# Optimization experiments

Measured on AMD Instinct MI355X. Metric: run time of the kernel, lower is better.

## Reference

```python
import jax, jax.numpy as jnp
import numpy as np


def setup_inputs() -> dict:
    key = jax.random.key(0)
    ks = jax.random.split(key, 8)
    B, D, H, W = 4, 96, 64, 64
    K, N, R = 4, 16, 6
    return {
        "x": jax.random.normal(ks[0], (B, D, H, W), jnp.float32),
        "x_proj_weight": jax.random.normal(ks[1], (K, R + 2 * N, D), jnp.float32) * 0.05,
        "dt_projs_weight": jax.random.normal(ks[2], (K, D, R), jnp.float32) * 0.1,
        "dt_projs_bias": jax.random.normal(ks[3], (K, D), jnp.float32) * 0.1,
        "A_logs": jax.random.uniform(ks[4], (K * D, N), jnp.float32),
        "Ds": jax.random.normal(ks[5], (K * D,), jnp.float32),
        "ln_weight": jnp.ones((D,), jnp.float32),
        "ln_bias": jnp.zeros((D,), jnp.float32),
    }


def reference(x, x_proj_weight, dt_projs_weight, dt_projs_bias, A_logs, Ds, ln_weight, ln_bias):
    B, D, H, W = x.shape
    K, _, R = dt_projs_weight.shape
    N = A_logs.shape[1]
    L = H * W

    # ---- CrossScan: 4 traversal orders (row-major, col-major, and their reverses) ----
    xf = x.reshape(B, D, L)                                   # row-major
    xt = jnp.transpose(x, (0, 1, 3, 2)).reshape(B, D, L)      # col-major
    xs = jnp.stack([xf, xt, xf[..., ::-1], xt[..., ::-1]], axis=1)  # (B, K, D, L)

    # ---- input-dependent projections ----
    x_dbl = jnp.einsum('bkdl,kcd->bkcl', xs, x_proj_weight)   # (B, K, R+2N, L)
    dts, Bs, Cs = jnp.split(x_dbl, [R, R + N], axis=2)        # Bs/Cs: (B, K, N, L)
    dts = jnp.einsum('bkrl,kdr->bkdl', dts, dt_projs_weight)  # (B, K, D, L)

    A = -jnp.exp(A_logs).reshape(K, D, N)                     # (K, D, N)
    delta = jax.nn.softplus(dts + dt_projs_bias[None, :, :, None])  # (B, K, D, L)

    # ---- selective (S6) scan over L ----
    def step(h, inp):
        d_t, u_t, B_t, C_t = inp  # (B,K,D) (B,K,D) (B,K,N) (B,K,N)
        dA = jnp.exp(d_t[..., None] * A[None])                # (B,K,D,N)
        h = h * dA + (d_t * u_t)[..., None] * B_t[:, :, None, :]
        y_t = jnp.einsum('bkdn,bkn->bkd', h, C_t)
        return h, y_t

    h0 = jnp.zeros((B, K, D, N), x.dtype)
    seq = (jnp.moveaxis(delta, -1, 0), jnp.moveaxis(xs, -1, 0),
           jnp.moveaxis(Bs, -1, 0), jnp.moveaxis(Cs, -1, 0))
    _, ys = jax.lax.scan(step, h0, seq)                       # (L, B, K, D)
    ys = jnp.moveaxis(ys, 0, -1)                              # (B, K, D, L)
    ys = ys + Ds.reshape(K, D)[None, :, :, None] * xs         # skip term D*u

    # ---- CrossMerge: undo the 4 traversal orders and sum ----
    m = ys[:, 0:2] + ys[:, 2:4][..., ::-1]                    # (B, 2, D, L)
    y = m[:, 0] + jnp.transpose(m[:, 1].reshape(B, D, W, H), (0, 1, 3, 2)).reshape(B, D, L)

    # ---- out_norm (LayerNorm over channels, v0 path) ----
    y = jnp.transpose(y, (0, 2, 1))                           # (B, L, D)
    mu = y.mean(-1, keepdims=True)
    var = y.var(-1, keepdims=True)
    y = (y - mu) / jnp.sqrt(var + 1e-5) * ln_weight + ln_bias
    return y.reshape(B, H, W, D)
```

## Files before the change

### kernel.cpp

```cpp
#include <hip/hip_runtime.h>
#include <hip/hip_fp16.h>
#include <math.h>

#define B_ 4
#define D_ 96
#define H_ 64
#define W_ 64
#define L_ 4096
#define K_ 4
#define N_ 16
#define R_ 6
#define C_ 38
#define SSX 128
#define CLSX (L_ / SSX)
#define CH_ (B_ * K_ * D_ * N_)

#if defined(__has_builtin)
#if __has_builtin(__builtin_amdgcn_exp2f)
#define EXP2F(x) __builtin_amdgcn_exp2f(x)
#else
#define EXP2F(x) exp2f(x)
#endif
#else
#define EXP2F(x) exp2f(x)
#endif
#define LOG2E 1.44269504f

#define SW(d) ((((d) >> 2) & 7) << 2)

__device__ __forceinline__ int src_idx(int k, int l) {
    int m = (k >= 2) ? (L_ - 1 - l) : l;
    if (k & 1) return ((m & 63) << 6) | (m >> 6);
    return m;
}

__device__ __forceinline__ float softplus_f(float a) {
    return (a > 15.f) ? a : __logf(1.f + __expf(a));
}

__device__ __forceinline__ ushort f2h(float v) {
    return __half_as_ushort(__float2half_rn(v));
}

__device__ __forceinline__ void load_h8(const __half* p, float* out) {
    uint4 raw = *(const uint4*)p;
    const __half2* h2 = (const __half2*)&raw;
#pragma unroll
    for (int i = 0; i < 4; ++i) {
        float2 f = __half22float2(h2[i]);
        out[2 * i] = f.x;
        out[2 * i + 1] = f.y;
    }
}

__device__ __forceinline__ void store_h8(__half* p, const float* v) {
    uint4 raw;
    __half2* h2 = (__half2*)&raw;
#pragma unroll
    for (int i = 0; i < 4; ++i)
        h2[i] = __floats2half2_rn(v[2 * i], v[2 * i + 1]);
    *(uint4*)p = raw;
}

__device__ __forceinline__ float4 load_h4(const __half* p) {
    uint2 raw = *(const uint2*)p;
    const __half2* h2 = (const __half2*)&raw;
    float2 a = __half22float2(h2[0]);
    float2 b = __half22float2(h2[1]);
    return make_float4(a.x, a.y, b.x, b.y);
}

__global__ __launch_bounds__(256) void transpose_kernel(
    const float* __restrict__ x,
    __half* __restrict__ xs2)
{
    int bid = blockIdx.x;
    int b = bid / (3 * 64);
    int rest = bid % (3 * 64);
    int dblk = rest / 64, lblk = rest % 64;
    int d0 = dblk * 32;
    int l0 = lblk * 64;
    int tid = threadIdx.x;

    __shared__ float s_t[32][65];

    for (int i = tid; i < 32 * 64; i += 256) {
        int d = i >> 6, l = i & 63;
        s_t[d][l] = x[((long)b * D_ + d0 + d) * L_ + l0 + l];
    }
    __syncthreads();

    for (int i = tid; i < 64 * 32; i += 256) {
        int l = i >> 5, d = i & 31;
        __half v = __float2half_rn(s_t[d][l]);
        xs2[((long)b * L_ + l0 + l) * D_ + d0 + d] = v;
        xs2[((long)(B_ + b) * L_ + l * 64 + lblk) * D_ + d0 + d] = v;
    }
}

__global__ __launch_bounds__(256) void proj_scan_kernel(
    const __half* __restrict__ xs2,
    const float* __restrict__ xpw,
    const float* __restrict__ wdt,
    const float* __restrict__ bdt,
    const float* __restrict__ A_logs,
    __half* __restrict__ delta,
    __half* __restrict__ Bsb,
    __half* __restrict__ Csb,
    __half* __restrict__ pAarr,
    __half* __restrict__ hharr)
{
    const int TL = 64;
    const int tiles = L_ / TL;
    int bid = blockIdx.x;
    int bk = bid / tiles;
    int tile = bid % tiles;
    int b = bk / K_, k = bk % K_;
    int l0 = tile * TL;
    int tid = threadIdx.x;

    __shared__ __align__(16) float  s_wpT[D_ * 40];
    __shared__ __align__(16) __half s_xs[D_ * 68];
    __shared__ __align__(16) float  s_wdt[R_ * D_];
    __shared__ __align__(16) float  s_bias[D_];
    __shared__ __align__(16) float  s_dts[R_ * 68];
    __shared__ __align__(16) float  s_B[TL * N_];

    for (int i = tid; i < C_ * D_; i += 256) {
        int d = i / C_, c = i % C_;
        int cp = (c < 6) ? c : c + 2;
        s_wpT[d * 40 + cp] = xpw[(k * C_ + c) * D_ + d];
    }
    for (int i = tid; i < 96; i += 256) {
        s_wpT[i * 40 + 6] = 0.f;
        s_wpT[i * 40 + 7] = 0.f;
    }
    for (int i = tid; i < R_ * D_; i += 256) {
        int r = i / D_, d = i % D_;
        s_wdt[i] = wdt[(k * D_ + d) * R_ + r];
    }
    if (tid < D_) s_bias[tid] = bdt[k * D_ + tid];

    const __half* xsp = xs2 + (long)((k & 1) * B_ + b) * L_ * D_;
    for (int i = tid; i < TL * 24; i += 256) {
        int lt = i / 24, dq = i % 24;
        int row = (k < 2) ? (l0 + lt) : (L_ - 1 - l0 - lt);
        uint2 raw = *(const uint2*)(xsp + (long)row * D_ + dq * 4);
        const __half* hv = (const __half*)&raw;
        int d0 = dq * 4;
        s_xs[(d0 + 0) * 68 + (lt ^ SW(d0 + 0))] = hv[0];
        s_xs[(d0 + 1) * 68 + (lt ^ SW(d0 + 1))] = hv[1];
        s_xs[(d0 + 2) * 68 + (lt ^ SW(d0 + 2))] = hv[2];
        s_xs[(d0 + 3) * 68 + (lt ^ SW(d0 + 3))] = hv[3];
    }
    __syncthreads();

    long base = (long)bk * L_ + l0;

    int ct = tid >> 4;
    int lt4 = (tid & 15) * 4;
    if (ct < 10) {
        int cp0 = ct * 4;
        float acc[4][4];
#pragma unroll
        for (int i = 0; i < 4; ++i)
#pragma unroll
            for (int j = 0; j < 4; ++j) acc[i][j] = 0.f;
#pragma unroll 4
        for (int d = 0; d < D_; ++d) {
            float4 wv = *(const float4*)(&s_wpT[d * 40 + cp0]);
            float4 xv = load_h4(&s_xs[d * 68 + (lt4 ^ SW(d))]);
            float wa[4] = {wv.x, wv.y, wv.z, wv.w};
            float xa[4] = {xv.x, xv.y, xv.z, xv.w};
#pragma unroll
            for (int ci = 0; ci < 4; ++ci)
#pragma unroll
                for (int li = 0; li < 4; ++li)
                    acc[ci][li] += wa[ci] * xa[li];
        }
        if (ct == 0) {
#pragma unroll
            for (int ci = 0; ci < 4; ++ci)
                *(float4*)(&s_dts[ci * 68 + lt4]) =
                    make_float4(acc[ci][0], acc[ci][1], acc[ci][2], acc[ci][3]);
        } else if (ct == 1) {
#pragma unroll
            for (int ci = 0; ci < 2; ++ci)
                *(float4*)(&s_dts[(4 + ci) * 68 + lt4]) =
                    make_float4(acc[ci][0], acc[ci][1], acc[ci][2], acc[ci][3]);
        } else if (ct < 6) {
            int n0 = cp0 - 8;
#pragma unroll
            for (int li = 0; li < 4; ++li) {
                ushort4 hv;
                hv.x = f2h(acc[0][li]); hv.y = f2h(acc[1][li]);
                hv.z = f2h(acc[2][li]); hv.w = f2h(acc[3][li]);
                *(ushort4*)(&Bsb[(base + lt4 + li) * N_ + n0]) = hv;
                *(float4*)(&s_B[(lt4 + li) * N_ + n0]) =
                    make_float4(acc[0][li], acc[1][li], acc[2][li], acc[3][li]);
            }
        } else {
            int n0 = cp0 - 24;
#pragma unroll
            for (int li = 0; li < 4; ++li) {
                ushort4 hv;
                hv.x = f2h(acc[0][li]); hv.y = f2h(acc[1][li]);
                hv.z = f2h(acc[2][li]); hv.w = f2h(acc[3][li]);
                *(ushort4*)(&Csb[(base + lt4 + li) * N_ + n0]) = hv;
            }
        }
    }
    __syncthreads();

    for (int tt = tid; tt < 24 * 16; tt += 256) {
        int dt = tt % 24, lt4b = (tt / 24) * 4;
        int d0 = dt * 4;
        float4 bias = *(const float4*)(&s_bias[d0]);
        float acc[4][4];
#pragma unroll
        for (int li = 0; li < 4; ++li) {
            acc[li][0] = bias.x; acc[li][1] = bias.y;
            acc[li][2] = bias.z; acc[li][3] = bias.w;
        }
#pragma unroll
        for (int r = 0; r < R_; ++r) {
            float4 wv = *(const float4*)(&s_wdt[r * D_ + d0]);
            float4 tv = *(const float4*)(&s_dts[r * 68 + lt4b]);
            float wa[4] = {wv.x, wv.y, wv.z, wv.w};
            float ta[4] = {tv.x, tv.y, tv.z, tv.w};
#pragma unroll
            for (int li = 0; li < 4; ++li)
#pragma unroll
                for (int di = 0; di < 4; ++di)
                    acc[li][di] += ta[li] * wa[di];
        }
#pragma unroll
        for (int li = 0; li < 4; ++li) {
            ushort4 o;
            o.x = f2h(softplus_f(acc[li][0]));
            o.y = f2h(softplus_f(acc[li][1]));
            o.z = f2h(softplus_f(acc[li][2]));
            o.w = f2h(softplus_f(acc[li][3]));
            *(ushort4*)(&delta[(base + lt4b + li) * D_ + d0]) = o;
        }
    }

    if (tid < 192) {
        int sub = tid / 96;
        int dd = tid % 96;
        int j = tile * 2 + sub;
        int kd = k * D_ + dd;

        float A2[16];
        {
            const float4* ap = (const float4*)(A_logs + kd * N_);
#pragma unroll
            for (int q = 0; q < 4; ++q) {
                float4 a = ap[q];
                A2[q * 4 + 0] = -__expf(a.x) * LOG2E;
                A2[q * 4 + 1] = -__expf(a.y) * LOG2E;
                A2[q * 4 + 2] = -__expf(a.z) * LOG2E;
                A2[q * 4 + 3] = -__expf(a.w) * LOG2E;
            }
        }
        float wdtr[R_];
#pragma unroll
        for (int r = 0; r < R_; ++r) wdtr[r] = s_wdt[r * D_ + dd];
        float biasv = s_bias[dd];
        int sw = SW(dd);

        float h[16];
#pragma unroll
        for (int i = 0; i < 16; ++i) h[i] = 0.f;
        float sdel = 0.f;

#pragma unroll 4
        for (int t = 0; t < CLSX; ++t) {
            int lt = sub * CLSX + t;
            float acc = biasv;
#pragma unroll
            for (int r = 0; r < R_; ++r) acc += wdtr[r] * s_dts[r * 68 + lt];
            float del = softplus_f(acc);
            float u = __half2float(s_xs[dd * 68 + (lt ^ sw)]);
            float Bv[16];
            *(float4*)(Bv + 0)  = *(const float4*)(&s_B[lt * N_ + 0]);
            *(float4*)(Bv + 4)  = *(const float4*)(&s_B[lt * N_ + 4]);
            *(float4*)(Bv + 8)  = *(const float4*)(&s_B[lt * N_ + 8]);
            *(float4*)(Bv + 12) = *(const float4*)(&s_B[lt * N_ + 12]);
            sdel += del;
            float delu = del * u;
#pragma unroll
            for (int i = 0; i < 16; ++i) {
                float dA = EXP2F(del * A2[i]);
                h[i] = h[i] * dA + delu * Bv[i];
            }
        }

        long sbase = (long)j * CH_ + (long)(bk * D_ + dd) * N_;
        float pv[16];
#pragma unroll
        for (int i = 0; i < 16; ++i) pv[i] = EXP2F(A2[i] * sdel);
        store_h8(pAarr + sbase, pv);
        store_h8(pAarr + sbase + 8, pv + 8);
        store_h8(hharr + sbase, h);
        store_h8(hharr + sbase + 8, h + 8);
    }
}

__global__ __launch_bounds__(256) void scan_combine(
    const __half* __restrict__ pAarr,
    __half* __restrict__ hharr)
{
    int c = blockIdx.x * 256 + threadIdx.x;
    float h = 0.f;
#pragma unroll 16
    for (int j = 0; j < SSX; ++j) {
        long idx = (long)j * CH_ + c;
        float tmp = __half2float(hharr[idx]);
        float pa  = __half2float(pAarr[idx]);
        hharr[idx] = __float2half_rn(h);
        h = tmp + pa * h;
    }
}

__global__ __launch_bounds__(384) void scan_part2_pair(
    const float* __restrict__ A_logs,
    const float* __restrict__ Ds,
    const __half* __restrict__ xs2,
    const __half* __restrict__ delta,
    const __half* __restrict__ Bsb,
    const __half* __restrict__ Csb,
    const __half* __restrict__ hharr,
    float* __restrict__ ypair)
{
    __shared__ float s_y[2][CLSX][D_];

    int bid = blockIdx.x;
    int b = bid / (2 * SSX);
    int rest = bid % (2 * SSX);
    int p = rest / SSX;
    int j = rest % SSX;
    int tid = threadIdx.x;
    int g = tid / 192;
    int r = tid % 192;
    int dd = r >> 1;
    int half = r & 1;
    int n0 = half * 8;

    int kdir = p + 2 * g;
    int bk = b * K_ + kdir;
    int jj = g ? (SSX - 1 - j) : j;
    int l0s = jj * CLSX;
    int kd = kdir * D_ + dd;

    float A2[8];
    {
        const float4* ap = (const float4*)(A_logs + kd * N_ + n0);
        float4 a0 = ap[0], a1 = ap[1];
        A2[0] = -__expf(a0.x) * LOG2E; A2[1] = -__expf(a0.y) * LOG2E;
        A2[2] = -__expf(a0.z) * LOG2E; A2[3] = -__expf(a0.w) * LOG2E;
        A2[4] = -__expf(a1.x) * LOG2E; A2[5] = -__expf(a1.y) * LOG2E;
        A2[6] = -__expf(a1.z) * LOG2E; A2[7] = -__expf(a1.w) * LOG2E;
    }
    float Dv = Ds[kd];

    const __half* dp = delta + ((long)bk * L_ + l0s) * D_ + dd;
    const __half* bp = Bsb + ((long)bk * L_ + l0s) * N_ + n0;
    const __half* cp = Csb + ((long)bk * L_ + l0s) * N_ + n0;
    const __half* xsp = xs2 + (long)(p * B_ + b) * L_ * D_;
    long urow0 = g ? ((long)j * CLSX + CLSX - 1) : (long)l0s;
    long ustep = g ? -D_ : D_;
    const __half* up = xsp + urow0 * D_ + dd;

    float h[8];
    load_h8(hharr + (long)jj * CH_ + (long)(bk * D_ + dd) * N_ + n0, h);

#pragma unroll 4
    for (int t = 0; t < CLSX; ++t) {
        float del = __half2float(dp[(long)t * D_]);
        float u   = __half2float(up[(long)t * ustep]);
        float Bv[8], Cv[8];
        load_h8(bp + t * N_, Bv);
        load_h8(cp + t * N_, Cv);
        float delu = del * u;
        float yv = 0.f;
#pragma unroll
        for (int i = 0; i < 8; ++i) {
            float dA = EXP2F(del * A2[i]);
            h[i] = h[i] * dA + delu * Bv[i];
            yv += h[i] * Cv[i];
        }
        yv += __shfl_xor(yv, 1);
        if (half == 0) {
            int tpos = g ? (CLSX - 1 - t) : t;
            s_y[g][tpos][dd] = yv + Dv * u;
        }
    }
    __syncthreads();

    float* yo = ypair + ((long)(p * B_ + b) * L_ + (long)j * CLSX) * D_;
    for (int i = tid; i < CLSX * 24; i += 384) {
        int lt = i / 24, dq = i % 24;
        int d0 = dq * 4;
        float4 o = make_float4(s_y[0][lt][d0 + 0] + s_y[1][lt][d0 + 0],
                               s_y[0][lt][d0 + 1] + s_y[1][lt][d0 + 1],
                               s_y[0][lt][d0 + 2] + s_y[1][lt][d0 + 2],
                               s_y[0][lt][d0 + 3] + s_y[1][lt][d0 + 3]);
        *(float4*)(yo + (long)lt * D_ + d0) = o;
    }
}

__global__ __launch_bounds__(256) void ln_merge_kernel(
    const float* __restrict__ ypair,
    const float* __restrict__ lnw,
    const float* __restrict__ lnb,
    float* __restrict__ out)
{
    int wid = (blockIdx.x * 256 + threadIdx.x) >> 6;
    int lane = threadIdx.x & 63;
    int b = wid / L_;
    int m = wid % L_;
    int mt = ((m & 63) << 6) | (m >> 6);

    const float* y0 = ypair + ((long)b * L_ + m) * D_;
    const float* y1 = ypair + ((long)(B_ + b) * L_ + mt) * D_;

    float v0 = y0[lane] + y1[lane];
    float v1 = (lane < 32) ? (y0[64 + lane] + y1[64 + lane]) : 0.f;

    float s  = v0 + v1;
    float s2 = v0 * v0 + v1 * v1;
#pragma unroll
    for (int mm = 1; mm < 64; mm <<= 1) {
        s  += __shfl_xor(s, mm);
        s2 += __shfl_xor(s2, mm);
    }
    float mu  = s * (1.f / D_);
    float var = s2 * (1.f / D_) - mu * mu;
    float rstd = rsqrtf(var + 1e-5f);

    long obase = (long)wid * D_;
    out[obase + lane] = (v0 - mu) * rstd * lnw[lane] + lnb[lane];
    if (lane < 32)
        out[obase + 64 + lane] = (v1 - mu) * rstd * lnw[64 + lane] + lnb[64 + lane];
}

__global__ __launch_bounds__(256) void proj_legacy(
    const float* __restrict__ x,
    const float* __restrict__ xpw,
    const float* __restrict__ wdt,
    const float* __restrict__ bdt,
    float* __restrict__ delta,
    float* __restrict__ Bsb,
    float* __restrict__ Csb)
{
    const int TL = 64;
    const int tiles = L_ / TL;
    int bid = blockIdx.x;
    int bk = bid / tiles;
    int tile = bid % tiles;
    int b = bk / K_, k = bk % K_;
    int l0 = tile * TL;
    int tid = threadIdx.x;

    __shared__ float s_wp[C_ * D_];
    __shared__ float s_wdt[R_ * D_];
    __shared__ float s_bias[D_];
    __shared__ float s_xs[D_ * (TL + 1)];
    __shared__ float s_xdbl[C_ * (TL + 1)];

    for (int i = tid; i < C_ * D_; i += 256) s_wp[i] = xpw[k * C_ * D_ + i];
    for (int i = tid; i < R_ * D_; i += 256) {
        int r = i / D_, d = i % D_;
        s_wdt[i] = wdt[(k * D_ + d) * R_ + r];
    }
    if (tid < D_) s_bias[tid] = bdt[k * D_ + tid];
    for (int i = tid; i < D_ * TL; i += 256) {
        int d = i / TL, lt = i % TL;
        s_xs[d * (TL + 1) + lt] = x[(b * D_ + d) * L_ + src_idx(k, l0 + lt)];
    }
    __syncthreads();

    for (int idx = tid; idx < C_ * TL; idx += 256) {
        int c = idx / TL, lt = idx % TL;
        const float* wr = &s_wp[c * D_];
        float acc = 0.f;
#pragma unroll 8
        for (int d = 0; d < D_; ++d) acc += wr[d] * s_xs[d * (TL + 1) + lt];
        s_xdbl[c * (TL + 1) + lt] = acc;
    }
    __syncthreads();

    long base = (long)bk * L_ + l0;
    for (int idx = tid; idx < TL * D_; idx += 256) {
        int lt = idx / D_, d = idx % D_;
        float acc = s_bias[d];
#pragma unroll
        for (int r = 0; r < R_; ++r)
            acc += s_wdt[r * D_ + d] * s_xdbl[r * (TL + 1) + lt];
        delta[(base + lt) * D_ + d] = softplus_f(acc);
    }
    for (int idx = tid; idx < TL * 2 * N_; idx += 256) {
        int lt = idx / (2 * N_), c2 = idx % (2 * N_);
        float v = s_xdbl[(R_ + c2) * (TL + 1) + lt];
        if (c2 < N_) Bsb[(base + lt) * N_ + c2] = v;
        else         Csb[(base + lt) * N_ + (c2 - N_)] = v;
    }
}

__global__ __launch_bounds__(64) void scan_serial(
    const float* __restrict__ x,
    const float* __restrict__ A_logs,
    const float* __restrict__ Ds,
    const float* __restrict__ delta,
    const float* __restrict__ Bsb,
    const float* __restrict__ Csb,
    float* __restrict__ ys)
{
    const int chans = D_ / 4;
    int bid = blockIdx.x;
    int bk = bid / chans;
    int d0 = (bid % chans) * 4;
    int b = bk / K_, k = bk % K_;
    int lane = threadIdx.x;
    int g = lane >> 4, n = lane & 15;
    int d = d0 + g;
    int kd = k * D_ + d;

    float A  = -__expf(A_logs[kd * N_ + n]);
    float Dv = Ds[kd];
    const float* dptr = delta + ((long)bk * L_) * D_ + d;
    const float* bptr = Bsb + (long)bk * L_ * N_ + n;
    const float* cptr = Csb + (long)bk * L_ * N_ + n;
    const float* xptr = x + ((long)b * D_ + d) * L_;
    float* yptr = ys + ((long)bk * L_) * D_ + d;

    float h = 0.f;
#pragma unroll 4
    for (int l = 0; l < L_; ++l) {
        float del = dptr[(long)l * D_];
        float u   = xptr[src_idx(k, l)];
        float Bt  = bptr[l * N_];
        float Ct  = cptr[l * N_];
        float dA  = __expf(del * A);
        h = h * dA + del * u * Bt;
        float yv = h * Ct;
        yv += __shfl_xor(yv, 1);
        yv += __shfl_xor(yv, 2);
        yv += __shfl_xor(yv, 4);
        yv += __shfl_xor(yv, 8);
        if (n == 0) yptr[(long)l * D_] = yv + Dv * u;
    }
}

__global__ __launch_bounds__(256) void merge_ln_kernel(
    const float* __restrict__ ys,
    const float* __restrict__ lnw,
    const float* __restrict__ lnb,
    float* __restrict__ out)
{
    int wid = (blockIdx.x * 256 + threadIdx.x) >> 6;
    int lane = threadIdx.x & 63;
    int b = wid / L_;
    int l = wid % L_;
    int lt = ((l & 63) << 6) | (l >> 6);

    long base0 = ((long)(b * K_ + 0) * L_ + l) * D_;
    long base2 = ((long)(b * K_ + 2) * L_ + (L_ - 1 - l)) * D_;
    long base1 = ((long)(b * K_ + 1) * L_ + lt) * D_;
    long base3 = ((long)(b * K_ + 3) * L_ + (L_ - 1 - lt)) * D_;

    int dA = lane;
    int dB = lane + 64;
    float v0 = ys[base0 + dA] + ys[base2 + dA] + ys[base1 + dA] + ys[base3 + dA];
    float v1 = 0.f;
    if (dB < D_)
        v1 = ys[base0 + dB] + ys[base2 + dB] + ys[base1 + dB] + ys[base3 + dB];

    float s  = v0 + v1;
    float s2 = v0 * v0 + v1 * v1;
#pragma unroll
    for (int m = 1; m < 64; m <<= 1) {
        s  += __shfl_xor(s, m);
        s2 += __shfl_xor(s2, m);
    }
    float mu  = s * (1.f / D_);
    float var = s2 * (1.f / D_) - mu * mu;
    float rstd = rsqrtf(var + 1e-5f);

    long obase = ((long)b * L_ + l) * D_;
    out[obase + dA] = (v0 - mu) * rstd * lnw[dA] + lnb[dA];
    if (dB < D_)
        out[obase + dB] = (v1 - mu) * rstd * lnw[dB] + lnb[dB];
}

extern "C" void kernel_launch(void* const* d_in, const int* in_sizes, int n_in,
                              void* d_out, int out_size, void* d_ws, size_t ws_size,
                              hipStream_t stream) {
    const float* x      = (const float*)d_in[0];
    const float* xpw    = (const float*)d_in[1];
    const float* wdt    = (const float*)d_in[2];
    const float* bdt    = (const float*)d_in[3];
    const float* A_logs = (const float*)d_in[4];
    const float* Ds     = (const float*)d_in[5];
    const float* lnw    = (const float*)d_in[6];
    const float* lnb    = (const float*)d_in[7];
    float* out = (float*)d_out;

    const long n_delta = (long)B_ * K_ * L_ * D_;
    const long n_bc    = (long)B_ * K_ * L_ * N_;
    const long n_bld   = (long)B_ * L_ * D_;
    const long n_sum   = (long)SSX * CH_;

    char* wsb = (char*)d_ws;
    __half* delta = (__half*)wsb;
    __half* Bsb   = (__half*)(wsb + n_delta * 2);
    __half* Csb   = (__half*)(wsb + n_delta * 2 + n_bc * 2);
    __half* xs2   = (__half*)(wsb + n_delta * 2 + n_bc * 4);
    float*  ypair = (float*)(wsb + n_delta * 2 + n_bc * 4 + 2 * n_bld * 2);
    __half* hharr = (__half*)((char*)ypair + 2 * n_bld * 4);
    __half* pAarr = (__half*)ypair;
    size_t need = (size_t)(n_delta * 2 + n_bc * 4 + 2 * n_bld * 2) +
                  (size_t)(2 * n_bld) * 4 + (size_t)n_sum * 2;

    if (ws_size >= need) {
        transpose_kernel<<<B_ * 3 * 64, 256, 0, stream>>>(x, xs2);
        proj_scan_kernel<<<B_ * K_ * (L_ / 64), 256, 0, stream>>>(
            xs2, xpw, wdt, bdt, A_logs, delta, Bsb, Csb, pAarr, hharr);
        scan_combine<<<CH_ / 256, 256, 0, stream>>>(pAarr, hharr);
        scan_part2_pair<<<B_ * 2 * SSX, 384, 0, stream>>>(
            A_logs, Ds, xs2, delta, Bsb, Csb, hharr, ypair);
        ln_merge_kernel<<<(B_ * L_) / 4, 256, 0, stream>>>(ypair, lnw, lnb, out);
    } else {
        float* ws = (float*)d_ws;
        float* deltaf = ws;
        float* Bsb2   = deltaf + n_delta;
        float* Csb2   = Bsb2 + n_bc;
        float* ys2    = Csb2 + n_bc;
        proj_legacy<<<B_ * K_ * (L_ / 64), 256, 0, stream>>>(
            x, xpw, wdt, bdt, deltaf, Bsb2, Csb2);
        scan_serial<<<B_ * K_ * (D_ / 4), 64, 0, stream>>>(
            x, A_logs, Ds, deltaf, Bsb2, Csb2, ys2);
        merge_ln_kernel<<<(B_ * L_) / 4, 256, 0, stream>>>(ys2, lnw, lnb, out);
    }
}
```

Measured before the change: 170.5 us.

## Split chunk-state combine into hierarchical three-pass scan and store ypair as fp16

The single serial combine kernel, which launched only 96 blocks each walking all 128 chunks, becomes three passes. The first reduces groups of 32 chunks into per-group (A, B) pairs. The second scans the four group pairs. The third replays each group from its prefix to write the chunk-start states. This raises block-level parallelism for the latency-bound combine, at the cost of an extra read pass over pAarr/hharr and two extra launches. Separately, the merged per-direction outputs (ypair) are stored in fp16 instead of fp32, halving that intermediate's write and read traffic in the scan and layer-norm kernels but adding rounding error before LayerNorm.

```diff
diff --git a/kernel.cpp b/kernel.cpp
--- a/kernel.cpp
+++ b/kernel.cpp
@@ -14,6 +14,8 @@
 #define SSX 128
 #define CLSX (L_ / SSX)
 #define CH_ (B_ * K_ * D_ * N_)
+#define GRP_ 4
+#define GJ_ (SSX / GRP_)
 
 #if defined(__has_builtin)
 #if __has_builtin(__builtin_amdgcn_exp2f)
@@ -307,19 +309,60 @@
     }
 }
 
-__global__ __launch_bounds__(256) void scan_combine(
+__global__ __launch_bounds__(256) void combine_c1(
     const __half* __restrict__ pAarr,
-    __half* __restrict__ hharr)
+    const __half* __restrict__ hharr,
+    float* __restrict__ gA,
+    float* __restrict__ gB)
+{
+    int g = blockIdx.x / 96;
+    int c = (blockIdx.x % 96) * 256 + threadIdx.x;
+    long base = (long)g * GJ_ * CH_ + c;
+    float A = 1.f, Bc = 0.f;
+#pragma unroll 8
+    for (int j = 0; j < GJ_; ++j) {
+        long idx = base + (long)j * CH_;
+        float a = __half2float(pAarr[idx]);
+        float b = __half2float(hharr[idx]);
+        A = a * A;
+        Bc = a * Bc + b;
+    }
+    gA[(long)g * CH_ + c] = A;
+    gB[(long)g * CH_ + c] = Bc;
+}
+
+__global__ __launch_bounds__(256) void combine_c2(
+    const float* __restrict__ gA,
+    float* __restrict__ gB)
 {
     int c = blockIdx.x * 256 + threadIdx.x;
     float h = 0.f;
-#pragma unroll 16
-    for (int j = 0; j < SSX; ++j) {
-        long idx = (long)j * CH_ + c;
-        float tmp = __half2float(hharr[idx]);
-        float pa  = __half2float(pAarr[idx]);
+#pragma unroll
+    for (int g = 0; g < GRP_; ++g) {
+        long idx = (long)g * CH_ + c;
+        float A = gA[idx];
+        float Bc = gB[idx];
+        gB[idx] = h;
+        h = A * h + Bc;
+    }
+}
+
+__global__ __launch_bounds__(256) void combine_c3(
+    const __half* __restrict__ pAarr,
+    const float* __restrict__ gB,
+    __half* __restrict__ hharr)
+{
+    int g = blockIdx.x / 96;
+    int c = (blockIdx.x % 96) * 256 + threadIdx.x;
+    long base = (long)g * GJ_ * CH_ + c;
+    float h = gB[(long)g * CH_ + c];
+#pragma unroll 8
+    for (int j = 0; j < GJ_; ++j) {
+        long idx = base + (long)j * CH_;
+        float a = __half2float(pAarr[idx]);
+        float b = __half2float(hharr[idx]);
         hharr[idx] = __float2half_rn(h);
-        h = tmp + pa * h;
+        h = b + a * h;
     }
 }
 
@@ -331,7 +374,7 @@
     const __half* __restrict__ Bsb,
     const __half* __restrict__ Csb,
     const __half* __restrict__ hharr,
-    float* __restrict__ ypair)
+    __half* __restrict__ ypair)
 {
     __shared__ float s_y[2][CLSX][D_];
 
@@ -398,20 +441,21 @@
     }
     __syncthreads();
 
-    float* yo = ypair + ((long)(p * B_ + b) * L_ + (long)j * CLSX) * D_;
+    __half* yo = ypair + ((long)(p * B_ + b) * L_ + (long)j * CLSX) * D_;
     for (int i = tid; i < CLSX * 24; i += 384) {
         int lt = i / 24, dq = i % 24;
         int d0 = dq * 4;
-        float4 o = make_float4(s_y[0][lt][d0 + 0] + s_y[1][lt][d0 + 0],
-                               s_y[0][lt][d0 + 1] + s_y[1][lt][d0 + 1],
-                               s_y[0][lt][d0 + 2] + s_y[1][lt][d0 + 2],
-                               s_y[0][lt][d0 + 3] + s_y[1][lt][d0 + 3]);
-        *(float4*)(yo + (long)lt * D_ + d0) = o;
+        ushort4 o;
+        o.x = f2h(s_y[0][lt][d0 + 0] + s_y[1][lt][d0 + 0]);
+        o.y = f2h(s_y[0][lt][d0 + 1] + s_y[1][lt][d0 + 1]);
+        o.z = f2h(s_y[0][lt][d0 + 2] + s_y[1][lt][d0 + 2]);
+        o.w = f2h(s_y[0][lt][d0 + 3] + s_y[1][lt][d0 + 3]);
+        *(ushort4*)(yo + (long)lt * D_ + d0) = o;
     }
 }
 
 __global__ __launch_bounds__(256) void ln_merge_kernel(
-    const float* __restrict__ ypair,
+    const __half* __restrict__ ypair,
     const float* __restrict__ lnw,
     const float* __restrict__ lnb,
     float* __restrict__ out)
@@ -422,11 +466,12 @@
     int m = wid % L_;
     int mt = ((m & 63) << 6) | (m >> 6);
 
-    const float* y0 = ypair + ((long)b * L_ + m) * D_;
-    const float* y1 = ypair + ((long)(B_ + b) * L_ + mt) * D_;
-
-    float v0 = y0[lane] + y1[lane];
-    float v1 = (lane < 32) ? (y0[64 + lane] + y1[64 + lane]) : 0.f;
+    const __half* y0 = ypair + ((long)b * L_ + m) * D_;
+    const __half* y1 = ypair + ((long)(B_ + b) * L_ + mt) * D_;
+
+    float v0 = __half2float(y0[lane]) + __half2float(y1[lane]);
+    float v1 = (lane < 32)
+        ? (__half2float(y0[64 + lane]) + __half2float(y1[64 + lane])) : 0.f;
 
     float s  = v0 + v1;
     float s2 = v0 * v0 + v1 * v1;
@@ -617,17 +662,22 @@
     __half* Bsb   = (__half*)(wsb + n_delta * 2);
     __half* Csb   = (__half*)(wsb + n_delta * 2 + n_bc * 2);
     __half* xs2   = (__half*)(wsb + n_delta * 2 + n_bc * 4);
-    float*  ypair = (float*)(wsb + n_delta * 2 + n_bc * 4 + 2 * n_bld * 2);
-    __half* hharr = (__half*)((char*)ypair + 2 * n_bld * 4);
+    __half* ypair = (__half*)(wsb + n_delta * 2 + n_bc * 4 + 2 * n_bld * 2);
+    __half* hharr = (__half*)((char*)ypair + 2 * n_bld * 2);
+    float*  gA    = (float*)((char*)hharr + n_sum * 2);
+    float*  gB    = gA + (long)GRP_ * CH_;
     __half* pAarr = (__half*)ypair;
-    size_t need = (size_t)(n_delta * 2 + n_bc * 4 + 2 * n_bld * 2) +
-                  (size_t)(2 * n_bld) * 4 + (size_t)n_sum * 2;
+    size_t need = (size_t)(n_delta * 2 + n_bc * 4 + 2 * n_bld * 2 +
+                           2 * n_bld * 2 + n_sum * 2) +
+                  (size_t)(2L * GRP_ * CH_) * 4;
 
     if (ws_size >= need) {
         transpose_kernel<<<B_ * 3 * 64, 256, 0, stream>>>(x, xs2);
         proj_scan_kernel<<<B_ * K_ * (L_ / 64), 256, 0, stream>>>(
             xs2, xpw, wdt, bdt, A_logs, delta, Bsb, Csb, pAarr, hharr);
-        scan_combine<<<CH_ / 256, 256, 0, stream>>>(pAarr, hharr);
+        combine_c1<<<GRP_ * 96, 256, 0, stream>>>(pAarr, hharr, gA, gB);
+        combine_c2<<<96, 256, 0, stream>>>(gA, gB);
+        combine_c3<<<GRP_ * 96, 256, 0, stream>>>(pAarr, gB, hharr);
         scan_part2_pair<<<B_ * 2 * SSX, 384, 0, stream>>>(
             A_logs, Ds, xs2, delta, Bsb, Csb, hharr, ypair);
         ln_merge_kernel<<<(B_ * L_) / 4, 256, 0, stream>>>(ypair, lnw, lnb, out);
```

Result: no change. 171.5 us (+0.6%).
